# Kernel optimization log

Hardware: AMD Instinct MI355X
Metric: run time of the kernel (lower is better)

## Reference

```python
import jax, jax.numpy as jnp
import numpy as np

EMB = 1024
FF = 4 * EMB

def _ternary(w):
    # BitNet b1.58 absmean quantization; forward uses pure ternary weights
    scale = jnp.maximum(jnp.mean(jnp.abs(w)), 1e-8)
    w_t = jnp.clip(jnp.round(w / scale), -1.0, 1.0)
    # STE: forward = w_t, backward = identity w.r.t. w
    return w + jax.lax.stop_gradient(w_t - w)

def setup_inputs() -> dict:
    key = jax.random.key(0)
    kx, k1, k2, kb1, kb2 = jax.random.split(key, 5)
    x = jax.random.normal(kx, (4, 2048, EMB), dtype=jnp.float32)
    # nn.Linear default init: U(-1/sqrt(fan_in), 1/sqrt(fan_in))
    lim1 = 1.0 / np.sqrt(EMB)
    lim2 = 1.0 / np.sqrt(FF)
    W1 = jax.random.uniform(k1, (FF, EMB), jnp.float32, -lim1, lim1)
    b1 = jax.random.uniform(kb1, (FF,), jnp.float32, -lim1, lim1)
    W2 = jax.random.uniform(k2, (EMB, FF), jnp.float32, -lim2, lim2)
    b2 = jax.random.uniform(kb2, (EMB,), jnp.float32, -lim2, lim2)
    return {"x": x, "W1": W1, "b1": b1, "W2": W2, "b2": b2}

def reference(x, W1, b1, W2, b2):
    h = jnp.einsum('bsd,fd->bsf', x, _ternary(W1)) + b1  # [B,S,FF]
    h = jax.nn.gelu(h, approximate=False)  # torch nn.GELU default = exact erf
    out = jnp.einsum('bsf,df->bsd', h, _ternary(W2)) + b2  # [B,S,EMB]
    return out
```

## Files before the change

### kernel.cpp

```cpp
#include <hip/hip_runtime.h>
#include <hip/hip_bf16.h>
#include <cstdint>
#include <cstddef>

typedef __bf16 bf16x8 __attribute__((ext_vector_type(8)));
typedef float  f32x4  __attribute__((ext_vector_type(4)));

__device__ __forceinline__ unsigned short f2bf(float f) {
    __hip_bfloat16 b = __float2bfloat16(f);
    return *reinterpret_cast<unsigned short*>(&b);
}

__device__ __forceinline__ float fast_gelu(float x) {
    float x2 = x * x;
    float m  = x * __builtin_fmaf(x2, -0.10294314f, -2.30220795f);
    float e  = __builtin_amdgcn_exp2f(m);
    return x * __builtin_amdgcn_rcpf(1.0f + e);
}


__global__ void abs_sum_cvt_kernel(const float4* __restrict__ w0, const float4* __restrict__ w1,
                                   int n4w, float* __restrict__ part,
                                   const float4* __restrict__ x, ushort4* __restrict__ xb,
                                   int n4x) {
    int seg = (int)blockIdx.x >> 9;
    int b = (int)blockIdx.x & 511;
    if (seg == 2) {
        for (int i = b * blockDim.x + threadIdx.x; i < n4x; i += 512 * blockDim.x) {
            float4 v = x[i];
            ushort4 o;
            o.x = f2bf(v.x); o.y = f2bf(v.y); o.z = f2bf(v.z); o.w = f2bf(v.w);
            xb[i] = o;
        }
        return;
    }
    const float4* w = seg ? w1 : w0;
    float s = 0.0f;
    for (int i = b * blockDim.x + threadIdx.x; i < n4w; i += 512 * blockDim.x) {
        float4 v = w[i];
        s += fabsf(v.x) + fabsf(v.y) + fabsf(v.z) + fabsf(v.w);
    }
    #pragma unroll
    for (int o = 32; o > 0; o >>= 1) s += __shfl_down(s, o, 64);
    __shared__ float ps[4];
    int lane = threadIdx.x & 63, wid = threadIdx.x >> 6;
    if (lane == 0) ps[wid] = s;
    __syncthreads();
    if (threadIdx.x == 0) part[blockIdx.x] = ps[0] + ps[1] + ps[2] + ps[3];
}

__global__ void ternarize_kernel(const float4* __restrict__ w0, ushort4* __restrict__ t0,
                                 const float4* __restrict__ w1, ushort4* __restrict__ t1,
                                 int n4w, const float* __restrict__ part, float inv_n) {
    int seg = (int)blockIdx.x >> 10;
    int b = (int)blockIdx.x & 1023;

    float s = 0.0f;
    for (int j = threadIdx.x; j < 512; j += 256) s += part[seg * 512 + j];
    #pragma unroll
    for (int o = 32; o > 0; o >>= 1) s += __shfl_down(s, o, 64);
    __shared__ float ps[4];
    __shared__ float sscale;
    int lane = threadIdx.x & 63, wid = threadIdx.x >> 6;
    if (lane == 0) ps[wid] = s;
    __syncthreads();
    if (threadIdx.x == 0) {
        float tot = ps[0] + ps[1] + ps[2] + ps[3];
        sscale = fmaxf(tot * inv_n, 1e-8f);
    }
    __syncthreads();
    float inv = 1.0f / sscale;

    const float4* w = seg ? w1 : w0;
    ushort4* t = seg ? t1 : t0;
    for (int i = b * blockDim.x + threadIdx.x; i < n4w; i += 1024 * blockDim.x) {
        float4 v = w[i];
        ushort4 o;
        o.x = f2bf(fminf(fmaxf(rintf(v.x * inv), -1.0f), 1.0f));
        o.y = f2bf(fminf(fmaxf(rintf(v.y * inv), -1.0f), 1.0f));
        o.z = f2bf(fminf(fmaxf(rintf(v.z * inv), -1.0f), 1.0f));
        o.w = f2bf(fminf(fmaxf(rintf(v.w * inv), -1.0f), 1.0f));
        t[i] = o;
    }
}


#define GLL(SRC, DST) __builtin_amdgcn_global_load_lds( \
    (const __attribute__((address_space(1))) void*)(SRC), \
    (__attribute__((address_space(3))) void*)(DST), 16, 0, 0)

#define BAR() do { asm volatile("" ::: "memory"); \
    __builtin_amdgcn_sched_barrier(0); \
    __builtin_amdgcn_s_barrier(); \
    __builtin_amdgcn_sched_barrier(0); \
    asm volatile("" ::: "memory"); } while (0)

#define WLG0() do { asm volatile("s_waitcnt lgkmcnt(0)" ::: "memory"); \
    __builtin_amdgcn_sched_barrier(0); } while (0)
#define WVM_N(NN) do { asm volatile("s_waitcnt vmcnt(" #NN ")" ::: "memory"); \
    __builtin_amdgcn_sched_barrier(0); } while (0)
#define WVM_TILE() do { if constexpr (SBL == 2) WVM_N(6); else WVM_N(5); } while (0)

#define LDA(MS, BUF) do { \
    _Pragma("unroll") \
    for (int f_ = 0; f_ < MF2; ++f_) { \
        const unsigned short* p_ = &As[(BUF)*16384 + AH*8192 + (rA0 + (MS)*(WM/2) + f_*16 + lr)*64]; \
        av[MS][f_][0] = *(const bf16x8*)(p_ + swz0); \
        av[MS][f_][1] = *(const bf16x8*)(p_ + swz1); \
    } \
} while (0)

#define LDB(NS, BUF) do { \
    _Pragma("unroll") \
    for (int g_ = 0; g_ < NF2; ++g_) { \
        const unsigned short* p_ = &Bs[(BUF)*(BN*64) + BHw*(BH*64) + (rB0 + (NS)*32 + g_*16 + lr)*64]; \
        bv[NS][g_][0] = *(const bf16x8*)(p_ + swz0); \
        bv[NS][g_][1] = *(const bf16x8*)(p_ + swz1); \
    } \
} while (0)

#define MMA(MS, NS) do { \
    __builtin_amdgcn_s_setprio(1); \
    _Pragma("unroll") \
    for (int f_ = 0; f_ < MF2; ++f_) { \
        _Pragma("unroll") \
        for (int g_ = 0; g_ < NF2; ++g_) { \
            acc[(MS)*MF2 + f_][(NS)*NF2 + g_] = __builtin_amdgcn_mfma_f32_16x16x32_bf16( \
                av[MS][f_][0], bv[NS][g_][0], acc[(MS)*MF2 + f_][(NS)*NF2 + g_], 0, 0, 0); \
            acc[(MS)*MF2 + f_][(NS)*NF2 + g_] = __builtin_amdgcn_mfma_f32_16x16x32_bf16( \
                av[MS][f_][1], bv[NS][g_][1], acc[(MS)*MF2 + f_][(NS)*NF2 + g_], 0, 0, 0); \
        } \
    } \
    __builtin_amdgcn_s_setprio(0); \
} while (0)

#define STAGE_A(BUF, H, T) do { \
    const unsigned short* s_ = pA + (size_t)((H)*128)*K + ((size_t)(T) << 6); \
    GLL(s_,                 &As[(BUF)*16384 + (H)*8192 + tid*8]); \
    GLL(s_ + (size_t)64*K,  &As[(BUF)*16384 + (H)*8192 + 4096 + tid*8]); \
} while (0)

#define STAGE_BH(BUF, H, T) do { \
    const unsigned short* s_ = pB + (size_t)((H)*BH)*K + ((size_t)(T) << 6); \
    GLL(s_, &Bs[(BUF)*(BN*64) + (H)*(BH*64) + tid*8]); \
    if constexpr (BN == 256) { \
        GLL(s_ + (size_t)64*K, &Bs[(BUF)*(BN*64) + (H)*(BH*64) + 4096 + tid*8]); \
    } \
} while (0)

template <int EPI, int K, int N, int BN, int WM>
__global__ __launch_bounds__(512, 2)
void gemm8p_kernel(const unsigned short* __restrict__ A,
                   const unsigned short* __restrict__ B,
                   const float* __restrict__ bias,
                   void* __restrict__ C) {
    constexpr int BM = 256;
    constexpr int WN = 64;
    constexpr int WARPS_N = BN / WN;
    constexpr int MF = WM / 16;
    constexpr int NF = WN / 16;
    constexpr int MF2 = MF / 2;
    constexpr int NF2 = NF / 2;
    constexpr int BH = (BN == 256) ? 128 : 64;
    constexpr int SBL = (BN == 256) ? 2 : 1;
    constexpr int KT = K / 64;
    constexpr int NBX = N / BN;
    static_assert((BM / WM) * WARPS_N == 8, "8 waves");
    static_assert(KT >= 4 && (KT & 1) == 0, "even KT >= 4");

    __shared__ __align__(16) unsigned short As[2 * 256 * 64];
    __shared__ __align__(16) unsigned short Bs[2 * BN * 64];

    const int tid  = threadIdx.x;
    const int lane = tid & 63;
    const int wid  = tid >> 6;
    const int lr = lane & 15;
    const int lq = lane >> 4;
    const int mb = wid / WARPS_N;
    const int nb = wid % WARPS_N;

    const int nwg = (int)gridDim.x;
    const int bid = (int)blockIdx.x;
    const int swz = (bid & 7) * (nwg >> 3) + (bid >> 3);
    const int bx = swz % NBX;
    const int by = swz / NBX;
    const size_t aRow0 = (size_t)by * BM;
    const size_t bRow0 = (size_t)bx * BN;

    const int sRow = tid >> 3;
    const int sChunk = ((tid & 7) ^ (sRow & 7)) << 3;
    const unsigned short* pA = A + (aRow0 + sRow) * (size_t)K + sChunk;
    const unsigned short* pB = B + (bRow0 + sRow) * (size_t)K + sChunk;

    const int swz0 = ((lq ^ (lr & 7)) << 3);
    const int swz1 = (((4 + lq) ^ (lr & 7)) << 3);
    const int AH  = (mb * WM) >> 7;
    const int rA0 = (mb * WM) & 127;
    const int BHw = (nb * WN) / BH;
    const int rB0 = (nb * WN) % BH;

    f32x4 acc[MF][NF];
    #pragma unroll
    for (int i_ = 0; i_ < MF; ++i_)
        #pragma unroll
        for (int j_ = 0; j_ < NF; ++j_)
            acc[i_][j_] = f32x4{0.f, 0.f, 0.f, 0.f};

    bf16x8 av[2][MF2][2];
    bf16x8 bv[2][NF2][2];

    STAGE_A(0, 0, 0); STAGE_A(0, 1, 0); STAGE_BH(0, 0, 0); STAGE_BH(0, 1, 0);
    STAGE_A(1, 0, 1); STAGE_A(1, 1, 1); STAGE_BH(1, 0, 1);
    WVM_TILE();
    BAR();

    #pragma unroll 1
    for (int it = 0; it < K / 128 - 1; ++it) {
        const int t1 = 2 * it + 1;
        const int t2 = 2 * it + 2;
        const int t3 = 2 * it + 3;

        LDA(0, 0); LDB(0, 0);
        STAGE_BH(1, 1, t1);
        BAR(); WLG0();
        MMA(0, 0);
        BAR();

        LDA(1, 0);
        BAR(); WLG0();
        MMA(1, 0);
        BAR();

        LDB(1, 0);
        STAGE_A(0, 0, t2); STAGE_A(0, 1, t2); STAGE_BH(0, 0, t2);
        BAR(); WLG0();
        MMA(1, 1); MMA(0, 1);
        WVM_TILE();
        BAR();

        LDA(0, 1); LDB(0, 1);
        STAGE_BH(0, 1, t2);
        BAR(); WLG0();
        MMA(0, 0);
        BAR();

        LDA(1, 1);
        BAR(); WLG0();
        MMA(1, 0);
        BAR();

        LDB(1, 1);
        STAGE_A(1, 0, t3); STAGE_A(1, 1, t3); STAGE_BH(1, 0, t3);
        BAR(); WLG0();
        MMA(1, 1); MMA(0, 1);
        WVM_TILE();
        BAR();
    }

    {
        LDA(0, 0); LDB(0, 0);
        STAGE_BH(1, 1, KT - 1);
        BAR(); WLG0();
        MMA(0, 0);
        BAR();

        LDA(1, 0);
        BAR(); WLG0();
        MMA(1, 0);
        BAR();

        LDB(1, 0);
        BAR(); WLG0();
        MMA(1, 1); MMA(0, 1);
        WVM_N(0);
        BAR();

        LDA(0, 1); LDB(0, 1);
        BAR(); WLG0();
        MMA(0, 0);
        BAR();

        LDA(1, 1);
        BAR(); WLG0();
        MMA(1, 0);
        BAR();

        LDB(1, 1);
        BAR(); WLG0();
        MMA(1, 1); MMA(0, 1);
    }

    #pragma unroll
    for (int mf = 0; mf < MF; ++mf) {
        #pragma unroll
        for (int nf = 0; nf < NF; ++nf) {
            const size_t col = bRow0 + (size_t)nb * WN + nf * 16 + lr;
            const float bvs = bias[col];
            #pragma unroll
            for (int r = 0; r < 4; ++r) {
                const size_t row = aRow0 + (size_t)mb * WM + mf * 16 + lq * 4 + r;
                float v = acc[mf][nf][r] + bvs;
                if constexpr (EPI == 0) {
                    ((unsigned short*)C)[row * (size_t)N + col] = f2bf(fast_gelu(v));
                } else {
                    ((float*)C)[row * (size_t)N + col] = v;
                }
            }
        }
    }
}

#undef GLL
#undef BAR
#undef WLG0
#undef WVM_N
#undef WVM_TILE
#undef LDA
#undef LDB
#undef MMA
#undef STAGE_A
#undef STAGE_BH


extern "C" void kernel_launch(void* const* d_in, const int* in_sizes, int n_in,
                              void* d_out, int out_size, void* d_ws, size_t ws_size,
                              hipStream_t stream) {
    const float* x  = (const float*)d_in[0];
    const float* W1 = (const float*)d_in[1];
    const float* b1 = (const float*)d_in[2];
    const float* W2 = (const float*)d_in[3];
    const float* b2 = (const float*)d_in[4];
    float* out = (float*)d_out;

    const int M = 8192, EMB = 1024, FF = 4096;
    const int nW = FF * EMB;

    char* ws = (char*)d_ws;
    float* part = (float*)ws;
    unsigned short* W1t = (unsigned short*)(ws + 16384);
    unsigned short* W2t = W1t + (size_t)nW;
    unsigned short* xb  = W2t + (size_t)nW;
    unsigned short* h   = xb  + (size_t)M * EMB;

    abs_sum_cvt_kernel<<<1536, 256, 0, stream>>>((const float4*)W1, (const float4*)W2,
                                                 nW / 4, part,
                                                 (const float4*)x, (ushort4*)xb,
                                                 (M * EMB) / 4);
    ternarize_kernel<<<2048, 256, 0, stream>>>((const float4*)W1, (ushort4*)W1t,
                                               (const float4*)W2, (ushort4*)W2t,
                                               nW / 4, part, 1.0f / nW);

    gemm8p_kernel<0, 1024, 4096, 256, 128><<<dim3(512), dim3(512), 0, stream>>>(xb, W1t, b1, h);
    gemm8p_kernel<1, 4096, 1024, 128, 64><<<dim3(256), dim3(512), 0, stream>>>(h, W2t, b2, out);
}
```

Baseline: 259.4 us.

## Fuse weight abs-sum and ternarize into one cooperative kernel keeping weights in registers

Merges the abs-sum/x-conversion kernel and the ternarize kernel into a single cooperative launch with a grid-wide sync. Each thread keeps its eight weight float4 values in registers across the sync, so the weights are read from global memory only once, and one kernel launch is removed. In exchange it relies on cooperative launch with 1024 blocks co-resident, pays the cost of a grid barrier, and uses more registers per thread.

```diff
diff --git a/kernel.cpp b/kernel.cpp
--- a/kernel.cpp
+++ b/kernel.cpp
@@ -1,7 +1,10 @@
 #include <hip/hip_runtime.h>
+#include <hip/hip_cooperative_groups.h>
 #include <hip/hip_bf16.h>
 #include <cstdint>
 #include <cstddef>
+
+namespace cg = cooperative_groups;
 
 typedef __bf16 bf16x8 __attribute__((ext_vector_type(8)));
 typedef float  f32x4  __attribute__((ext_vector_type(4)));
@@ -19,68 +22,69 @@
 }
 
 
-__global__ void abs_sum_cvt_kernel(const float4* __restrict__ w0, const float4* __restrict__ w1,
-                                   int n4w, float* __restrict__ part,
-                                   const float4* __restrict__ x, ushort4* __restrict__ xb,
-                                   int n4x) {
-    int seg = (int)blockIdx.x >> 9;
-    int b = (int)blockIdx.x & 511;
-    if (seg == 2) {
-        for (int i = b * blockDim.x + threadIdx.x; i < n4x; i += 512 * blockDim.x) {
-            float4 v = x[i];
-            ushort4 o;
-            o.x = f2bf(v.x); o.y = f2bf(v.y); o.z = f2bf(v.z); o.w = f2bf(v.w);
-            xb[i] = o;
-        }
-        return;
-    }
+__global__ __launch_bounds__(256, 4)
+void aux_fused_kernel(const float4* __restrict__ w0, const float4* __restrict__ w1,
+                      ushort4* __restrict__ t0, ushort4* __restrict__ t1,
+                      float* __restrict__ part, float inv_n,
+                      const float4* __restrict__ x, ushort4* __restrict__ xb,
+                      int n4x) {
+    const int b   = (int)blockIdx.x;
+    const int seg = b >> 9;
+    const int bb  = b & 511;
+    const int tid = (int)threadIdx.x;
+    const int lane = tid & 63, wid = tid >> 6;
+
+    __shared__ float ps[4];
+    __shared__ float sscale;
+
     const float4* w = seg ? w1 : w0;
+    const int base = bb * 256 + tid;
+    float4 vreg[8];
     float s = 0.0f;
-    for (int i = b * blockDim.x + threadIdx.x; i < n4w; i += 512 * blockDim.x) {
-        float4 v = w[i];
+    #pragma unroll
+    for (int j = 0; j < 8; ++j) {
+        float4 v = w[base + j * 131072];
+        vreg[j] = v;
         s += fabsf(v.x) + fabsf(v.y) + fabsf(v.z) + fabsf(v.w);
     }
     #pragma unroll
     for (int o = 32; o > 0; o >>= 1) s += __shfl_down(s, o, 64);
-    __shared__ float ps[4];
-    int lane = threadIdx.x & 63, wid = threadIdx.x >> 6;
     if (lane == 0) ps[wid] = s;
     __syncthreads();
-    if (threadIdx.x == 0) part[blockIdx.x] = ps[0] + ps[1] + ps[2] + ps[3];
-}
-
-__global__ void ternarize_kernel(const float4* __restrict__ w0, ushort4* __restrict__ t0,
-                                 const float4* __restrict__ w1, ushort4* __restrict__ t1,
-                                 int n4w, const float* __restrict__ part, float inv_n) {
-    int seg = (int)blockIdx.x >> 10;
-    int b = (int)blockIdx.x & 1023;
-
-    float s = 0.0f;
-    for (int j = threadIdx.x; j < 512; j += 256) s += part[seg * 512 + j];
-    #pragma unroll
-    for (int o = 32; o > 0; o >>= 1) s += __shfl_down(s, o, 64);
-    __shared__ float ps[4];
-    __shared__ float sscale;
-    int lane = threadIdx.x & 63, wid = threadIdx.x >> 6;
-    if (lane == 0) ps[wid] = s;
+    if (tid == 0) part[b] = ps[0] + ps[1] + ps[2] + ps[3];
+
+    for (int i = b * 256 + tid; i < n4x; i += 1024 * 256) {
+        float4 v = x[i];
+        ushort4 o4;
+        o4.x = f2bf(v.x); o4.y = f2bf(v.y); o4.z = f2bf(v.z); o4.w = f2bf(v.w);
+        xb[i] = o4;
+    }
+
+    cg::this_grid().sync();
+
+    float s2 = 0.0f;
+    for (int j = tid; j < 512; j += 256) s2 += part[seg * 512 + j];
+    #pragma unroll
+    for (int o = 32; o > 0; o >>= 1) s2 += __shfl_down(s2, o, 64);
+    if (lane == 0) ps[wid] = s2;
     __syncthreads();
-    if (threadIdx.x == 0) {
+    if (tid == 0) {
         float tot = ps[0] + ps[1] + ps[2] + ps[3];
         sscale = fmaxf(tot * inv_n, 1e-8f);
     }
     __syncthreads();
-    float inv = 1.0f / sscale;
-
-    const float4* w = seg ? w1 : w0;
+    const float inv = 1.0f / sscale;
+
     ushort4* t = seg ? t1 : t0;
-    for (int i = b * blockDim.x + threadIdx.x; i < n4w; i += 1024 * blockDim.x) {
-        float4 v = w[i];
-        ushort4 o;
-        o.x = f2bf(fminf(fmaxf(rintf(v.x * inv), -1.0f), 1.0f));
-        o.y = f2bf(fminf(fmaxf(rintf(v.y * inv), -1.0f), 1.0f));
-        o.z = f2bf(fminf(fmaxf(rintf(v.z * inv), -1.0f), 1.0f));
-        o.w = f2bf(fminf(fmaxf(rintf(v.w * inv), -1.0f), 1.0f));
-        t[i] = o;
+    #pragma unroll
+    for (int j = 0; j < 8; ++j) {
+        float4 v = vreg[j];
+        ushort4 o4;
+        o4.x = f2bf(fminf(fmaxf(rintf(v.x * inv), -1.0f), 1.0f));
+        o4.y = f2bf(fminf(fmaxf(rintf(v.y * inv), -1.0f), 1.0f));
+        o4.z = f2bf(fminf(fmaxf(rintf(v.z * inv), -1.0f), 1.0f));
+        o4.w = f2bf(fminf(fmaxf(rintf(v.w * inv), -1.0f), 1.0f));
+        t[base + j * 131072] = o4;
     }
 }
 
@@ -342,13 +346,20 @@
     unsigned short* xb  = W2t + (size_t)nW;
     unsigned short* h   = xb  + (size_t)M * EMB;
 
-    abs_sum_cvt_kernel<<<1536, 256, 0, stream>>>((const float4*)W1, (const float4*)W2,
-                                                 nW / 4, part,
-                                                 (const float4*)x, (ushort4*)xb,
-                                                 (M * EMB) / 4);
-    ternarize_kernel<<<2048, 256, 0, stream>>>((const float4*)W1, (ushort4*)W1t,
-                                               (const float4*)W2, (ushort4*)W2t,
-                                               nW / 4, part, 1.0f / nW);
+    {
+        const float4* w0p = (const float4*)W1;
+        const float4* w1p = (const float4*)W2;
+        ushort4* t0p = (ushort4*)W1t;
+        ushort4* t1p = (ushort4*)W2t;
+        float* partp = part;
+        float inv_n = 1.0f / nW;
+        const float4* xp = (const float4*)x;
+        ushort4* xbp = (ushort4*)xb;
+        int n4x = (M * EMB) / 4;
+        void* args[] = {&w0p, &w1p, &t0p, &t1p, &partp, &inv_n, &xp, &xbp, &n4x};
+        hipLaunchCooperativeKernel((const void*)aux_fused_kernel,
+                                   dim3(1024), dim3(256), args, 0, stream);
+    }
 
     gemm8p_kernel<0, 1024, 4096, 256, 128><<<dim3(512), dim3(512), 0, stream>>>(xb, W1t, b1, h);
     gemm8p_kernel<1, 4096, 1024, 128, 64><<<dim3(256), dim3(512), 0, stream>>>(h, W2t, b2, out);
```

Result: slower. 361.7 us (+39.4%).
